# Kernel tuning notes

Measured on AMD Instinct MI355X. Metric: run time of the kernel, lower is better.

Reference implementation:

```python
import jax, jax.numpy as jnp
import numpy as np

HEAD_DIM = 64
SCALE = HEAD_DIM ** -0.5
NUM_HEADS = 16


def setup_inputs() -> dict:
    key = jax.random.key(0)
    k1, k2, k3, k4 = jax.random.split(key, 4)
    dim = 1024
    query = jax.random.normal(k1, (8, 512, dim), dtype=jnp.float32)
    memory = jax.random.normal(k2, (8, 512, dim), dtype=jnp.float32)
    # nn.Linear weights are [out, in]; scale like default init
    W_Q = jax.random.normal(k3, (dim, dim), dtype=jnp.float32) * (dim ** -0.5)
    W_K = jax.random.normal(k4, (dim, dim), dtype=jnp.float32) * (dim ** -0.5)
    return {"query": query, "memory": memory, "W_Q": W_Q, "W_K": W_K}


def reference(query, memory, W_Q, W_K):
    # Q: [K, Lq, E], K: [B, Lk, E]  (E = H * D)
    Q = query @ W_Q.T
    Km = memory @ W_K.T
    Kb, Lq, E = Q.shape
    Bb, Lk, _ = Km.shape
    Qh = Q.reshape(Kb, Lq, NUM_HEADS, HEAD_DIM).transpose(0, 2, 1, 3)  # K H q D
    Kh = Km.reshape(Bb, Lk, NUM_HEADS, HEAD_DIM).transpose(0, 2, 1, 3)  # B H k D
    # logits: [B, K, H, q, k]
    logits = jnp.einsum('ahqd,bhkd->bahqk', Qh, Kh) * SCALE
    energies = jax.nn.logsumexp(logits, axis=-2) / SCALE  # [B, K, H, k]
    energies = energies.mean(axis=1)  # [B, H, k]
    return energies
```

## Files before the change

### kernel.cpp

```cpp
#include <hip/hip_runtime.h>
#include <hip/hip_bf16.h>

typedef short short8 __attribute__((ext_vector_type(8)));
typedef float f32x4 __attribute__((ext_vector_type(4)));
typedef unsigned short u16;

__device__ __forceinline__ unsigned short f2bf(float f) {
  unsigned int u = __float_as_uint(f);
  u += 0x7fffu + ((u >> 16) & 1u);
  return (unsigned short)(u >> 16);
}

__device__ __forceinline__ void glds16(const void* g, void* l) {
  __builtin_amdgcn_global_load_lds(
      (const __attribute__((address_space(1))) unsigned int*)g,
      (__attribute__((address_space(3))) unsigned int*)l, 16, 0, 0);
}

__global__ __launch_bounds__(256) void prep(const float4* __restrict__ q,
                                            const float4* __restrict__ m,
                                            const float4* __restrict__ wq,
                                            const float4* __restrict__ wk,
                                            ushort4* __restrict__ qb,
                                            ushort4* __restrict__ mb,
                                            ushort4* __restrict__ wqb,
                                            ushort4* __restrict__ wkb,
                                            float4* __restrict__ out0) {
  const int i = blockIdx.x * 256 + threadIdx.x;
  const float c = 0.18033688011112042f;
  if (i < 1048576) {
    float4 v = q[i];
    ushort4 o; o.x = f2bf(v.x); o.y = f2bf(v.y); o.z = f2bf(v.z); o.w = f2bf(v.w);
    qb[i] = o;
  } else if (i < 2097152) {
    float4 v = m[i - 1048576];
    ushort4 o; o.x = f2bf(v.x); o.y = f2bf(v.y); o.z = f2bf(v.z); o.w = f2bf(v.w);
    mb[i - 1048576] = o;
  } else if (i < 2359296) {
    float4 v = wq[i - 2097152];
    ushort4 o; o.x = f2bf(v.x * c); o.y = f2bf(v.y * c); o.z = f2bf(v.z * c); o.w = f2bf(v.w * c);
    wqb[i - 2097152] = o;
  } else if (i < 2621440) {
    float4 v = wk[i - 2359296];
    ushort4 o; o.x = f2bf(v.x); o.y = f2bf(v.y); o.z = f2bf(v.z); o.w = f2bf(v.w);
    wkb[i - 2359296] = o;
  } else if (i < 2637824) {
    out0[i - 2621440] = (float4){0.f, 0.f, 0.f, 0.f};
  }
}

__global__ __launch_bounds__(256) void gemm_bt2(const u16* __restrict__ A0,
                                                const u16* __restrict__ B0,
                                                u16* __restrict__ C0,
                                                const u16* __restrict__ A1,
                                                const u16* __restrict__ B1,
                                                u16* __restrict__ C1) {
  __shared__ u16 As[128 * 64];
  __shared__ u16 Bs[128 * 64];
  const u16* A = blockIdx.z ? A1 : A0;
  const u16* B = blockIdx.z ? B1 : B0;
  u16* C = blockIdx.z ? C1 : C0;
  const int t = threadIdx.x;
  const int lane = t & 63, wave = t >> 6;
  const int l15 = lane & 15, quad = lane >> 4;
  const int mb = blockIdx.y * 128, nb = blockIdx.x * 128;
  const int wm = (wave & 1) * 64, wn = (wave >> 1) * 64;

  const int srow = lane >> 3;
  const int scol = ((lane & 7) ^ srow) * 8;

  f32x4 acc[4][4];
#pragma unroll
  for (int i = 0; i < 4; i++)
#pragma unroll
    for (int j = 0; j < 4; j++) acc[i][j] = (f32x4){0.f, 0.f, 0.f, 0.f};

  for (int kb = 0; kb < 1024; kb += 64) {
#pragma unroll
    for (int j = 0; j < 4; j++) {
      const int mi_ = wave * 4 + j;
      const int row = mi_ * 8 + srow;
      glds16(A + (size_t)(mb + row) * 1024 + kb + scol, &As[mi_ * 512 + lane * 8]);
      glds16(B + (size_t)(nb + row) * 1024 + kb + scol, &Bs[mi_ * 512 + lane * 8]);
    }
    __syncthreads();
#pragma unroll
    for (int kk = 0; kk < 2; kk++) {
      const int cb = kk * 4;
      const int sw = l15 & 7;
      short8 af[4], bfr[4];
#pragma unroll
      for (int mi = 0; mi < 4; mi++)
        af[mi] = *(const short8*)&As[(wm + mi * 16 + l15) * 64 + ((cb + quad) ^ sw) * 8];
#pragma unroll
      for (int ni = 0; ni < 4; ni++)
        bfr[ni] = *(const short8*)&Bs[(wn + ni * 16 + l15) * 64 + ((cb + quad) ^ sw) * 8];
#pragma unroll
      for (int mi = 0; mi < 4; mi++)
#pragma unroll
        for (int ni = 0; ni < 4; ni++)
          acc[mi][ni] = __builtin_amdgcn_mfma_f32_16x16x32_bf16(
              af[mi], bfr[ni], acc[mi][ni], 0, 0, 0);
    }
    __syncthreads();
  }
#pragma unroll
  for (int mi = 0; mi < 4; mi++)
#pragma unroll
    for (int r = 0; r < 4; r++) {
      const int row = mb + wm + mi * 16 + quad * 4 + r;
      const size_t base = (size_t)row * 1024 + nb + wn;
#pragma unroll
      for (int ni = 0; ni < 4; ni++)
        C[base + ni * 16 + l15] = f2bf(acc[mi][ni][r]);
    }
}

__global__ __launch_bounds__(256) void attn_lse2(const u16* __restrict__ Qp,
                                                 const u16* __restrict__ Kp,
                                                 float* __restrict__ out) {
  __shared__ u16 qs[64 * 64];
  const int t = threadIdx.x;
  const int lane = t & 63, wave = t >> 6;
  const int l15 = lane & 15, quad = lane >> 4;
  const int kt = blockIdx.x & 1, aa = blockIdx.x >> 1;
  const int h = blockIdx.y, b = blockIdx.z;
  const int kwave = kt * 256 + wave * 64;

  short8 klo[4], khi[4];
#pragma unroll
  for (int tt = 0; tt < 4; tt++) {
    const short8* kg = (const short8*)(Kp + (size_t)(b * 512 + kwave + tt * 16 + l15) * 1024
                                       + h * 64 + quad * 8);
    klo[tt] = kg[0];
    khi[tt] = kg[4];
  }

  const int srow = lane >> 3;
  const int scol = ((lane & 7) ^ srow) * 8;
  const u16* qbase = Qp + (size_t)(aa * 512) * 1024 + h * 64;

  float cs0 = 0.f, cs1 = 0.f, cs2 = 0.f, cs3 = 0.f;

  for (int q0 = 0; q0 < 512; q0 += 64) {
    __syncthreads();
#pragma unroll
    for (int j = 0; j < 2; j++) {
      const int mi_ = wave * 2 + j;
      const int row = q0 + mi_ * 8 + srow;
      glds16(qbase + (size_t)row * 1024 + scol, &qs[mi_ * 512 + lane * 8]);
    }
    __syncthreads();
#pragma unroll
    for (int qt = 0; qt < 4; qt++) {
      const int rbase = (qt * 16 + l15) * 64;
      const int sw = l15 & 7;
      short8 alo = *(const short8*)&qs[rbase + (quad ^ sw) * 8];
      short8 ahi = *(const short8*)&qs[rbase + ((4 + quad) ^ sw) * 8];
      f32x4 ac0 = (f32x4){0.f, 0.f, 0.f, 0.f};
      f32x4 ac1 = ac0, ac2 = ac0, ac3 = ac0;
      ac0 = __builtin_amdgcn_mfma_f32_16x16x32_bf16(alo, klo[0], ac0, 0, 0, 0);
      ac0 = __builtin_amdgcn_mfma_f32_16x16x32_bf16(ahi, khi[0], ac0, 0, 0, 0);
      ac1 = __builtin_amdgcn_mfma_f32_16x16x32_bf16(alo, klo[1], ac1, 0, 0, 0);
      ac1 = __builtin_amdgcn_mfma_f32_16x16x32_bf16(ahi, khi[1], ac1, 0, 0, 0);
      ac2 = __builtin_amdgcn_mfma_f32_16x16x32_bf16(alo, klo[2], ac2, 0, 0, 0);
      ac2 = __builtin_amdgcn_mfma_f32_16x16x32_bf16(ahi, khi[2], ac2, 0, 0, 0);
      ac3 = __builtin_amdgcn_mfma_f32_16x16x32_bf16(alo, klo[3], ac3, 0, 0, 0);
      ac3 = __builtin_amdgcn_mfma_f32_16x16x32_bf16(ahi, khi[3], ac3, 0, 0, 0);
#pragma unroll
      for (int r = 0; r < 4; r++) {
        cs0 += exp2f(ac0[r]);
        cs1 += exp2f(ac1[r]);
        cs2 += exp2f(ac2[r]);
        cs3 += exp2f(ac3[r]);
      }
    }
  }
  cs0 += __shfl_xor(cs0, 16); cs0 += __shfl_xor(cs0, 32);
  cs1 += __shfl_xor(cs1, 16); cs1 += __shfl_xor(cs1, 32);
  cs2 += __shfl_xor(cs2, 16); cs2 += __shfl_xor(cs2, 32);
  cs3 += __shfl_xor(cs3, 16); cs3 += __shfl_xor(cs3, 32);
  const float v = quad == 0 ? cs0 : quad == 1 ? cs1 : quad == 2 ? cs2 : cs3;
  atomicAdd(out + (size_t)b * 8192 + h * 512 + kwave + quad * 16 + l15, __logf(v));
}

extern "C" void kernel_launch(void* const* d_in, const int* in_sizes, int n_in,
                              void* d_out, int out_size, void* d_ws, size_t ws_size,
                              hipStream_t stream) {
  const float* query  = (const float*)d_in[0];
  const float* memory = (const float*)d_in[1];
  const float* wq     = (const float*)d_in[2];
  const float* wk     = (const float*)d_in[3];
  float* out = (float*)d_out;

  char* ws = (char*)d_ws;
  const size_t MB = 1024 * 1024;
  u16* qb  = (u16*)(ws);
  u16* mb_ = (u16*)(ws + 8  * MB);
  u16* wqb = (u16*)(ws + 16 * MB);
  u16* wkb = (u16*)(ws + 18 * MB);
  u16* Qp  = (u16*)(ws + 20 * MB);
  u16* Kp  = (u16*)(ws + 28 * MB);

  prep<<<10304, 256, 0, stream>>>((const float4*)query, (const float4*)memory,
                                  (const float4*)wq, (const float4*)wk,
                                  (ushort4*)qb, (ushort4*)mb_, (ushort4*)wqb,
                                  (ushort4*)wkb, (float4*)d_out);
  gemm_bt2<<<dim3(8, 32, 2), 256, 0, stream>>>(qb, wqb, Qp, mb_, wkb, Kp);
  attn_lse2<<<dim3(16, 16, 8), 256, 0, stream>>>(Qp, Kp, out);
}
```

Before: 177.1 us.

## Emit GEMM output in MFMA fragment layout and double-buffer GEMM LDS

The projection GEMM now writes Q and K directly in a per-head, per-16-row MFMA fragment order, so the attention kernel can load operands straight from global memory with contiguous 16-byte loads. This removes the LDS staging and barriers from the attention loop. The GEMM moves to 512 threads with double-buffered LDS, prefetching the next K-slice before computing the current one, and the attention kernel uses the raw exp2 builtin. The scattered fragment-order stores from the GEMM epilogue may coalesce less well, and the doubled LDS footprint may reduce occupancy.

Result: faster. 171.5 us (-3.1%).

```diff
diff --git a/kernel.cpp b/kernel.cpp
--- a/kernel.cpp
+++ b/kernel.cpp
@@ -49,131 +49,139 @@
   }
 }
 
-__global__ __launch_bounds__(256) void gemm_bt2(const u16* __restrict__ A0,
-                                                const u16* __restrict__ B0,
-                                                u16* __restrict__ C0,
-                                                const u16* __restrict__ A1,
-                                                const u16* __restrict__ B1,
-                                                u16* __restrict__ C1) {
-  __shared__ u16 As[128 * 64];
-  __shared__ u16 Bs[128 * 64];
+__global__ __launch_bounds__(512) void gemm_frag(const u16* __restrict__ A0,
+                                                 const u16* __restrict__ B0,
+                                                 u16* __restrict__ F0,
+                                                 const u16* __restrict__ A1,
+                                                 const u16* __restrict__ B1,
+                                                 u16* __restrict__ F1) {
+  __shared__ u16 As[2][128 * 64];
+  __shared__ u16 Bs[2][128 * 64];
   const u16* A = blockIdx.z ? A1 : A0;
   const u16* B = blockIdx.z ? B1 : B0;
-  u16* C = blockIdx.z ? C1 : C0;
+  u16* F = blockIdx.z ? F1 : F0;
   const int t = threadIdx.x;
   const int lane = t & 63, wave = t >> 6;
   const int l15 = lane & 15, quad = lane >> 4;
   const int mb = blockIdx.y * 128, nb = blockIdx.x * 128;
-  const int wm = (wave & 1) * 64, wn = (wave >> 1) * 64;
+  const int wm = (wave & 1) * 64;
+  const int wn = (wave >> 1) * 32;
 
   const int srow = lane >> 3;
   const int scol = ((lane & 7) ^ srow) * 8;
 
-  f32x4 acc[4][4];
+  f32x4 acc[4][2];
 #pragma unroll
   for (int i = 0; i < 4; i++)
 #pragma unroll
-    for (int j = 0; j < 4; j++) acc[i][j] = (f32x4){0.f, 0.f, 0.f, 0.f};
-
-  for (int kb = 0; kb < 1024; kb += 64) {
-#pragma unroll
-    for (int j = 0; j < 4; j++) {
-      const int mi_ = wave * 4 + j;
-      const int row = mi_ * 8 + srow;
-      glds16(A + (size_t)(mb + row) * 1024 + kb + scol, &As[mi_ * 512 + lane * 8]);
-      glds16(B + (size_t)(nb + row) * 1024 + kb + scol, &Bs[mi_ * 512 + lane * 8]);
-    }
+    for (int j = 0; j < 2; j++) acc[i][j] = (f32x4){0.f, 0.f, 0.f, 0.f};
+
+#pragma unroll
+  for (int j = 0; j < 2; j++) {
+    const int g = wave * 2 + j;
+    glds16(A + (size_t)(mb + g * 8 + srow) * 1024 + scol, &As[0][g * 512 + lane * 8]);
+    glds16(B + (size_t)(nb + g * 8 + srow) * 1024 + scol, &Bs[0][g * 512 + lane * 8]);
+  }
+
+  const int sw = l15 & 7;
+  for (int it = 0; it < 16; ++it) {
     __syncthreads();
+    if (it < 15) {
+      const int kb = (it + 1) * 64, bf_ = (it + 1) & 1;
+#pragma unroll
+      for (int j = 0; j < 2; j++) {
+        const int g = wave * 2 + j;
+        glds16(A + (size_t)(mb + g * 8 + srow) * 1024 + kb + scol, &As[bf_][g * 512 + lane * 8]);
+        glds16(B + (size_t)(nb + g * 8 + srow) * 1024 + kb + scol, &Bs[bf_][g * 512 + lane * 8]);
+      }
+    }
+    const u16* as = As[it & 1];
+    const u16* bs = Bs[it & 1];
 #pragma unroll
     for (int kk = 0; kk < 2; kk++) {
       const int cb = kk * 4;
-      const int sw = l15 & 7;
-      short8 af[4], bfr[4];
+      short8 af[4], bfr[2];
 #pragma unroll
       for (int mi = 0; mi < 4; mi++)
-        af[mi] = *(const short8*)&As[(wm + mi * 16 + l15) * 64 + ((cb + quad) ^ sw) * 8];
-#pragma unroll
-      for (int ni = 0; ni < 4; ni++)
-        bfr[ni] = *(const short8*)&Bs[(wn + ni * 16 + l15) * 64 + ((cb + quad) ^ sw) * 8];
+        af[mi] = *(const short8*)&as[(wm + mi * 16 + l15) * 64 + ((cb + quad) ^ sw) * 8];
+#pragma unroll
+      for (int ni = 0; ni < 2; ni++)
+        bfr[ni] = *(const short8*)&bs[(wn + ni * 16 + l15) * 64 + ((cb + quad) ^ sw) * 8];
 #pragma unroll
       for (int mi = 0; mi < 4; mi++)
 #pragma unroll
-        for (int ni = 0; ni < 4; ni++)
+        for (int ni = 0; ni < 2; ni++)
           acc[mi][ni] = __builtin_amdgcn_mfma_f32_16x16x32_bf16(
               af[mi], bfr[ni], acc[mi][ni], 0, 0, 0);
     }
-    __syncthreads();
-  }
-#pragma unroll
-  for (int mi = 0; mi < 4; mi++)
+  }
+
+  const int dt_hi = ((wave >> 1) & 1) * 2;
+#pragma unroll
+  for (int mi = 0; mi < 4; mi++) {
 #pragma unroll
     for (int r = 0; r < 4; r++) {
       const int row = mb + wm + mi * 16 + quad * 4 + r;
-      const size_t base = (size_t)row * 1024 + nb + wn;
-#pragma unroll
-      for (int ni = 0; ni < 4; ni++)
-        C[base + ni * 16 + l15] = f2bf(acc[mi][ni][r]);
-    }
-}
-
-__global__ __launch_bounds__(256) void attn_lse2(const u16* __restrict__ Qp,
-                                                 const u16* __restrict__ Kp,
+      const int bt = row >> 9;
+      const int t16 = (row >> 4) & 31;
+      const int m15 = quad * 4 + r;
+#pragma unroll
+      for (int ni = 0; ni < 2; ni++) {
+        const int col = nb + wn + ni * 16 + l15;
+        const int h = col >> 6;
+        const int dt = dt_hi + ni;
+        const int half = dt >> 1;
+        const int quadF = ((dt & 1) << 1) + (l15 >> 3);
+        const int j = l15 & 7;
+        const size_t idx = ((size_t)((bt * 16 + h) * 32 + t16) << 10)
+                         + (half << 9) + (((quadF << 4) + m15) << 3) + j;
+        F[idx] = f2bf(acc[mi][ni][r]);
+      }
+    }
+  }
+}
+
+__global__ __launch_bounds__(256) void attn_lse3(const u16* __restrict__ Qf,
+                                                 const u16* __restrict__ Kf,
                                                  float* __restrict__ out) {
-  __shared__ u16 qs[64 * 64];
   const int t = threadIdx.x;
   const int lane = t & 63, wave = t >> 6;
   const int l15 = lane & 15, quad = lane >> 4;
-  const int kt = blockIdx.x & 1, aa = blockIdx.x >> 1;
+  const int aa = blockIdx.x >> 1, khalf = blockIdx.x & 1;
   const int h = blockIdx.y, b = blockIdx.z;
-  const int kwave = kt * 256 + wave * 64;
+  const int tt0 = khalf * 16 + wave * 4;
 
   short8 klo[4], khi[4];
 #pragma unroll
   for (int tt = 0; tt < 4; tt++) {
-    const short8* kg = (const short8*)(Kp + (size_t)(b * 512 + kwave + tt * 16 + l15) * 1024
-                                       + h * 64 + quad * 8);
-    klo[tt] = kg[0];
-    khi[tt] = kg[4];
-  }
-
-  const int srow = lane >> 3;
-  const int scol = ((lane & 7) ^ srow) * 8;
-  const u16* qbase = Qp + (size_t)(aa * 512) * 1024 + h * 64;
+    const u16* kp = Kf + (((size_t)(b * 16 + h) * 32 + tt0 + tt) << 10) + lane * 8;
+    klo[tt] = *(const short8*)kp;
+    khi[tt] = *(const short8*)(kp + 512);
+  }
+
+  const u16* qp = Qf + (((size_t)(aa * 16 + h) * 32) << 10) + lane * 8;
 
   float cs0 = 0.f, cs1 = 0.f, cs2 = 0.f, cs3 = 0.f;
-
-  for (int q0 = 0; q0 < 512; q0 += 64) {
-    __syncthreads();
-#pragma unroll
-    for (int j = 0; j < 2; j++) {
-      const int mi_ = wave * 2 + j;
-      const int row = q0 + mi_ * 8 + srow;
-      glds16(qbase + (size_t)row * 1024 + scol, &qs[mi_ * 512 + lane * 8]);
-    }
-    __syncthreads();
-#pragma unroll
-    for (int qt = 0; qt < 4; qt++) {
-      const int rbase = (qt * 16 + l15) * 64;
-      const int sw = l15 & 7;
-      short8 alo = *(const short8*)&qs[rbase + (quad ^ sw) * 8];
-      short8 ahi = *(const short8*)&qs[rbase + ((4 + quad) ^ sw) * 8];
-      f32x4 ac0 = (f32x4){0.f, 0.f, 0.f, 0.f};
-      f32x4 ac1 = ac0, ac2 = ac0, ac3 = ac0;
-      ac0 = __builtin_amdgcn_mfma_f32_16x16x32_bf16(alo, klo[0], ac0, 0, 0, 0);
-      ac0 = __builtin_amdgcn_mfma_f32_16x16x32_bf16(ahi, khi[0], ac0, 0, 0, 0);
-      ac1 = __builtin_amdgcn_mfma_f32_16x16x32_bf16(alo, klo[1], ac1, 0, 0, 0);
-      ac1 = __builtin_amdgcn_mfma_f32_16x16x32_bf16(ahi, khi[1], ac1, 0, 0, 0);
-      ac2 = __builtin_amdgcn_mfma_f32_16x16x32_bf16(alo, klo[2], ac2, 0, 0, 0);
-      ac2 = __builtin_amdgcn_mfma_f32_16x16x32_bf16(ahi, khi[2], ac2, 0, 0, 0);
-      ac3 = __builtin_amdgcn_mfma_f32_16x16x32_bf16(alo, klo[3], ac3, 0, 0, 0);
-      ac3 = __builtin_amdgcn_mfma_f32_16x16x32_bf16(ahi, khi[3], ac3, 0, 0, 0);
-#pragma unroll
-      for (int r = 0; r < 4; r++) {
-        cs0 += exp2f(ac0[r]);
-        cs1 += exp2f(ac1[r]);
-        cs2 += exp2f(ac2[r]);
-        cs3 += exp2f(ac3[r]);
-      }
+#pragma unroll 4
+  for (int qt = 0; qt < 32; ++qt, qp += 1024) {
+    short8 alo = *(const short8*)qp;
+    short8 ahi = *(const short8*)(qp + 512);
+    f32x4 ac0 = (f32x4){0.f, 0.f, 0.f, 0.f};
+    f32x4 ac1 = ac0, ac2 = ac0, ac3 = ac0;
+    ac0 = __builtin_amdgcn_mfma_f32_16x16x32_bf16(alo, klo[0], ac0, 0, 0, 0);
+    ac0 = __builtin_amdgcn_mfma_f32_16x16x32_bf16(ahi, khi[0], ac0, 0, 0, 0);
+    ac1 = __builtin_amdgcn_mfma_f32_16x16x32_bf16(alo, klo[1], ac1, 0, 0, 0);
+    ac1 = __builtin_amdgcn_mfma_f32_16x16x32_bf16(ahi, khi[1], ac1, 0, 0, 0);
+    ac2 = __builtin_amdgcn_mfma_f32_16x16x32_bf16(alo, klo[2], ac2, 0, 0, 0);
+    ac2 = __builtin_amdgcn_mfma_f32_16x16x32_bf16(ahi, khi[2], ac2, 0, 0, 0);
+    ac3 = __builtin_amdgcn_mfma_f32_16x16x32_bf16(alo, klo[3], ac3, 0, 0, 0);
+    ac3 = __builtin_amdgcn_mfma_f32_16x16x32_bf16(ahi, khi[3], ac3, 0, 0, 0);
+#pragma unroll
+    for (int r = 0; r < 4; r++) {
+      cs0 += __builtin_amdgcn_exp2f(ac0[r]);
+      cs1 += __builtin_amdgcn_exp2f(ac1[r]);
+      cs2 += __builtin_amdgcn_exp2f(ac2[r]);
+      cs3 += __builtin_amdgcn_exp2f(ac3[r]);
     }
   }
   cs0 += __shfl_xor(cs0, 16); cs0 += __shfl_xor(cs0, 32);
@@ -181,7 +189,8 @@
   cs2 += __shfl_xor(cs2, 16); cs2 += __shfl_xor(cs2, 32);
   cs3 += __shfl_xor(cs3, 16); cs3 += __shfl_xor(cs3, 32);
   const float v = quad == 0 ? cs0 : quad == 1 ? cs1 : quad == 2 ? cs2 : cs3;
-  atomicAdd(out + (size_t)b * 8192 + h * 512 + kwave + quad * 16 + l15, __logf(v));
+  atomicAdd(out + (size_t)b * 8192 + h * 512 + khalf * 256 + wave * 64 + quad * 16 + l15,
+            __logf(v));
 }
 
 extern "C" void kernel_launch(void* const* d_in, const int* in_sizes, int n_in,
@@ -199,13 +208,13 @@
   u16* mb_ = (u16*)(ws + 8  * MB);
   u16* wqb = (u16*)(ws + 16 * MB);
   u16* wkb = (u16*)(ws + 18 * MB);
-  u16* Qp  = (u16*)(ws + 20 * MB);
-  u16* Kp  = (u16*)(ws + 28 * MB);
+  u16* Qf  = (u16*)(ws + 20 * MB);
+  u16* Kf  = (u16*)(ws + 28 * MB);
 
   prep<<<10304, 256, 0, stream>>>((const float4*)query, (const float4*)memory,
                                   (const float4*)wq, (const float4*)wk,
                                   (ushort4*)qb, (ushort4*)mb_, (ushort4*)wqb,
                                   (ushort4*)wkb, (float4*)d_out);
-  gemm_bt2<<<dim3(8, 32, 2), 256, 0, stream>>>(qb, wqb, Qp, mb_, wkb, Kp);
-  attn_lse2<<<dim3(16, 16, 8), 256, 0, stream>>>(Qp, Kp, out);
-}
+  gemm_frag<<<dim3(8, 32, 2), 512, 0, stream>>>(qb, wqb, Qf, mb_, wkb, Kf);
+  attn_lse3<<<dim3(16, 16, 8), 256, 0, stream>>>(Qf, Kf, out);
+}
```
